# Optimization experiments

Measured on AMD Instinct MI355X. Metric: run time of the kernel, lower is better.

The kernel has to match this reference:

```python
import jax, jax.numpy as jnp
import numpy as np

N, E, IN, HID, H, G, OUT = 50000, 800000, 128, 96, 8, 64, 10
D = HID // H  # per-head dim = 12


def setup_inputs() -> dict:
    key = jax.random.key(0)
    ks = jax.random.split(key, 24)
    s = 0.1
    inp = {
        'x': jax.random.normal(ks[0], (N, IN), jnp.float32),
        'src': jax.random.randint(ks[1], (E,), 0, N, jnp.int32),
        'dst': jax.random.randint(ks[2], (E,), 0, N, jnp.int32),
        'graph_id': jax.random.randint(ks[3], (N,), 0, G, jnp.int32),
        # GraphConv layers (norm='both', weight + bias)
        'W1': jax.random.normal(ks[4], (IN, HID), jnp.float32) * s,
        'b1': jnp.zeros((HID,), jnp.float32),
        'W2': jax.random.normal(ks[5], (HID, HID), jnp.float32) * s,
        'b2': jnp.zeros((HID,), jnp.float32),
        # 3 GATv2 layers, stacked params
        'Ws': jax.random.normal(ks[6], (3, HID, HID), jnp.float32) * s,
        'bs': jnp.zeros((3, HID), jnp.float32),
        'Wd': jax.random.normal(ks[7], (3, HID, HID), jnp.float32) * s,
        'bd': jnp.zeros((3, HID), jnp.float32),
        'attn': jax.random.normal(ks[8], (3, H, D), jnp.float32) * s,
        # classifier MLP (dropout is identity at inference)
        'Wc1': jax.random.normal(ks[9], (HID, HID), jnp.float32) * s,
        'bc1': jnp.zeros((HID,), jnp.float32),
        'Wc2': jax.random.normal(ks[10], (HID, HID // 2), jnp.float32) * s,
        'bc2': jnp.zeros((HID // 2,), jnp.float32),
        'Wc3': jax.random.normal(ks[11], (HID // 2, OUT), jnp.float32) * s,
        'bc3': jnp.zeros((OUT,), jnp.float32),
    }
    return inp


def _graph_conv(h, W, b, src, dst):
    # DGL GraphConv, norm='both', allow_zero_in_degree (degrees clamped to >=1)
    ones = jnp.ones((E,), h.dtype)
    deg_out = jnp.clip(jax.ops.segment_sum(ones, src, N), 1.0)
    deg_in = jnp.clip(jax.ops.segment_sum(ones, dst, N), 1.0)
    h = (h * (deg_out ** -0.5)[:, None]) @ W          # [N, out]
    agg = jax.ops.segment_sum(h[src], dst, N)          # sum over in-edges
    return agg * (deg_in ** -0.5)[:, None] + b


def _gatv2(h, Ws, bs, Wd, bd, attn, src, dst):
    fs = (h @ Ws + bs).reshape(N, H, D)
    fd = (h @ Wd + bd).reshape(N, H, D)
    e = jax.nn.leaky_relu(fs[src] + fd[dst], 0.2)      # [E, H, D]
    logits = jnp.einsum('ehd,hd->eh', e, attn)         # [E, H]
    # edge softmax over incoming edges of each dst node
    m = jax.ops.segment_max(logits, dst, N)            # [N, H]
    ex = jnp.exp(logits - m[dst])
    den = jax.ops.segment_sum(ex, dst, N)              # [N, H]
    a = ex / den[dst]                                  # [E, H]
    rst = jax.ops.segment_sum(a[:, :, None] * fs[src], dst, N)  # [N, H, D]
    return jax.nn.relu(rst).reshape(N, HID)            # activation=relu, then view


def reference(x, src, dst, graph_id, W1, b1, W2, b2, Ws, bs, Wd, bd, attn,
              Wc1, bc1, Wc2, bc2, Wc3, bc3):
    h = jax.nn.relu(_graph_conv(x, W1, b1, src, dst))
    h = jax.nn.relu(_graph_conv(h, W2, b2, src, dst))
    for i in range(3):
        h = _gatv2(h, Ws[i], bs[i], Wd[i], bd[i], attn[i], src, dst)
    # dgl.max_nodes: per-graph max readout
    hg = jax.ops.segment_max(h, graph_id, G)           # [G, HID]
    z = jax.nn.relu(hg @ Wc1 + bc1)
    z = jax.nn.relu(z @ Wc2 + bc2)
    return z @ Wc3 + bc3                               # [G, OUT]
```

## Files before the change

kernel.cpp:

```cpp
#include <hip/hip_runtime.h>
#include <hip/hip_bf16.h>

#define Nn 50000
#define Ee 800000
#define INF_ 128
#define HIDF 96
#define HH 8
#define DD 12
#define GG 64
#define OUTF 10

#define SCAN_CHUNK 512
#define SCAN_BLOCKS ((Nn + SCAN_CHUNK - 1) / SCAN_CHUNK)
#define NSB ((Nn + 255) / 256)
#define RB 128

#define HCHK 256
#define HCHKE (Ee / HCHK)
#define NW 12512
#define DBIN 64

__global__ __launch_bounds__(512) void hist_lds(const int* __restrict__ src,
                                                const int* __restrict__ dst,
                                                unsigned int* __restrict__ partS,
                                                unsigned int* __restrict__ partD,
                                                unsigned char* __restrict__ edge_slot) {
    __shared__ unsigned int hS[NW];
    __shared__ unsigned int hD[NW];
    int b = blockIdx.x, t = threadIdx.x;
    for (int i = t; i < NW; i += 512) { hS[i] = 0u; hD[i] = 0u; }
    __syncthreads();
    int base = b * HCHKE;
    for (int i = t; i < HCHKE; i += 512) {
        int d = dst[base + i];
        unsigned int old = atomicAdd(&hD[d >> 2], 1u << ((d & 3) * 8));
        edge_slot[base + i] = (unsigned char)((old >> ((d & 3) * 8)) & 0xFFu);
        int s = src[base + i];
        atomicAdd(&hS[s >> 2], 1u << ((s & 3) * 8));
    }
    __syncthreads();
    for (int i = t; i < NW; i += 512) {
        partD[(size_t)b * NW + i] = hD[i];
        partS[(size_t)b * NW + i] = hS[i];
    }
}

__global__ __launch_bounds__(256) void hist_scan(unsigned int* __restrict__ partD,
                                                 const unsigned int* __restrict__ partS,
                                                 int* __restrict__ cnt_in,
                                                 float* __restrict__ degI_is,
                                                 float* __restrict__ degO_is,
                                                 int* __restrict__ dcnt) {
    __shared__ int hbin[DBIN];
    int t = threadIdx.x;
    if (t < DBIN) hbin[t] = 0;
    __syncthreads();
    int w = blockIdx.x * 256 + t;
    if (w < NW) {
        unsigned int run = 0u, totS = 0u;
        for (int b = 0; b < HCHK; ++b) {
            size_t idx = (size_t)b * NW + w;
            unsigned int v = partD[idx];
            partD[idx] = run;
            run += v;
            totS += partS[idx];
        }
#pragma unroll
        for (int j = 0; j < 4; ++j) {
            int k = w * 4 + j;
            if (k < Nn) {
                int di = (int)((run >> (j * 8)) & 0xFFu);
                int dо = (int)((totS >> (j * 8)) & 0xFFu);
                cnt_in[k] = di;
                degI_is[k] = rsqrtf((float)max(di, 1));
                degO_is[k] = rsqrtf((float)max(dо, 1));
                atomicAdd(&hbin[DBIN - 1 - min(di, DBIN - 1)], 1);
            }
        }
    }
    __syncthreads();
    if (t < DBIN && hbin[t]) atomicAdd(&dcnt[t], hbin[t]);
}

__global__ __launch_bounds__(256) void scan1_kernel(const int* __restrict__ cnt,
                                                    int* __restrict__ row_start,
                                                    int* __restrict__ blk_sum, int N) {
    __shared__ int part[256];
    int t = threadIdx.x;
    int base = blockIdx.x * SCAN_CHUNK;
    int i0 = base + 2 * t, i1 = i0 + 1;
    int a = (i0 < N) ? cnt[i0] : 0;
    int b = (i1 < N) ? cnt[i1] : 0;
    int s = a + b;
    part[t] = s;
    __syncthreads();
    for (int off = 1; off < 256; off <<= 1) {
        int v = (t >= off) ? part[t - off] : 0;
        __syncthreads();
        part[t] += v;
        __syncthreads();
    }
    int excl = part[t] - s;
    if (i0 < N) row_start[i0] = excl;
    if (i1 < N) row_start[i1] = excl + a;
    if (t == 255) blk_sum[blockIdx.x] = part[255];
}

__global__ __launch_bounds__(128) void scan2_kernel(const int* __restrict__ blk_sum,
                                                    int* __restrict__ blk_off,
                                                    int* __restrict__ row_start,
                                                    const int* __restrict__ dcnt,
                                                    int* __restrict__ dcur, int N) {
    __shared__ int part[128];
    int t = threadIdx.x;
    if (blockIdx.x == 0) {
        int v0 = (t < SCAN_BLOCKS) ? blk_sum[t] : 0;
        part[t] = v0;
        __syncthreads();
        for (int off = 1; off < 128; off <<= 1) {
            int v = (t >= off) ? part[t - off] : 0;
            __syncthreads();
            part[t] += v;
            __syncthreads();
        }
        blk_off[t] = part[t] - v0;
        if (t == 127) row_start[N] = part[127];
    } else {
        int v0 = (t < DBIN) ? dcnt[t] : 0;
        part[t] = v0;
        __syncthreads();
        for (int off = 1; off < DBIN; off <<= 1) {
            int v = (t >= off) ? part[t - off] : 0;
            __syncthreads();
            part[t] += v;
            __syncthreads();
        }
        if (t < DBIN) dcur[t] = part[t] - v0;
    }
}

__global__ __launch_bounds__(256) void scan3_kernel(int* __restrict__ row_start,
                                                    const int* __restrict__ blk_off,
                                                    const int* __restrict__ cnt_in,
                                                    int* __restrict__ dcur,
                                                    int* __restrict__ perm, int N) {
    int t = threadIdx.x;
    if (blockIdx.x < SCAN_BLOCKS) {
        int base = blockIdx.x * SCAN_CHUNK;
        int off = blk_off[blockIdx.x];
        int i0 = base + 2 * t, i1 = i0 + 1;
        if (i0 < N) row_start[i0] += off;
        if (i1 < N) row_start[i1] += off;
    } else {
        __shared__ int lh[DBIN];
        __shared__ int lbase[DBIN];
        if (t < DBIN) lh[t] = 0;
        __syncthreads();
        int n = (blockIdx.x - SCAN_BLOCKS) * 256 + t;
        int bin = 0, lslot = 0;
        if (n < N) {
            bin = DBIN - 1 - min(cnt_in[n], DBIN - 1);
            lslot = atomicAdd(&lh[bin], 1);
        }
        __syncthreads();
        if (t < DBIN) lbase[t] = lh[t] ? atomicAdd(&dcur[t], lh[t]) : 0;
        __syncthreads();
        if (n < N) perm[lbase[bin] + lslot] = n;
    }
}

__global__ __launch_bounds__(512) void fill_kernel(const int* __restrict__ src,
                                                   const int* __restrict__ dst,
                                                   const int* __restrict__ row_start,
                                                   const unsigned int* __restrict__ partD,
                                                   const unsigned char* __restrict__ edge_slot,
                                                   int* __restrict__ csr_src) {
    int b = blockIdx.x, t = threadIdx.x;
    int base = b * HCHKE;
    size_t po = (size_t)b * NW;
    for (int i = t; i < HCHKE; i += 512) {
        int e = base + i;
        int d = dst[e];
        int cb = (int)((partD[po + (d >> 2)] >> ((d & 3) * 8)) & 0xFFu);
        csr_src[row_start[d] + cb + (int)edge_slot[e]] = src[e];
    }
}

__global__ __launch_bounds__(192, 1) void gemm96(const float* __restrict__ A, int K,
                                                 const float* __restrict__ W,
                                                 const float* __restrict__ bias,
                                                 const float* __restrict__ rowScale,
                                                 float* __restrict__ out, int N) {
    __shared__ float W_lds[128 * 96];
    const int t = threadIdx.x;
    const int row0 = blockIdx.x * 64;
    const int tcol = t % 24;
    const int trow = t / 24;

    for (int i = t; i < K * 24; i += 192)
        ((float4*)W_lds)[i] = ((const float4*)W)[i];

    const float* Ap[8];
    float sc[8];
#pragma unroll
    for (int i = 0; i < 8; ++i) {
        int gr = row0 + trow + 8 * i;
        gr = gr < N ? gr : N - 1;
        Ap[i] = A + (size_t)gr * K;
        sc[i] = rowScale ? rowScale[gr] : 1.f;
    }
    float acc[8][4];
#pragma unroll
    for (int i = 0; i < 8; ++i)
#pragma unroll
        for (int j = 0; j < 4; ++j) acc[i][j] = 0.f;

    float4 bufA[8], bufB[8];
#pragma unroll
    for (int i = 0; i < 8; ++i) bufA[i] = *((const float4*)(Ap[i]));

    __syncthreads();

    auto compute = [&](const float4* a, int k) {
#pragma unroll
        for (int kk = 0; kk < 4; ++kk) {
            float4 wv = *((const float4*)(W_lds + (k + kk) * 96 + tcol * 4));
#pragma unroll
            for (int i = 0; i < 8; ++i) {
                float av = ((kk == 0) ? a[i].x : (kk == 1) ? a[i].y
                           : (kk == 2) ? a[i].z : a[i].w) * sc[i];
                acc[i][0] = fmaf(av, wv.x, acc[i][0]);
                acc[i][1] = fmaf(av, wv.y, acc[i][1]);
                acc[i][2] = fmaf(av, wv.z, acc[i][2]);
                acc[i][3] = fmaf(av, wv.w, acc[i][3]);
            }
        }
    };

    for (int k = 0; k + 8 <= K; k += 8) {
#pragma unroll
        for (int i = 0; i < 8; ++i) bufB[i] = *((const float4*)(Ap[i] + k + 4));
        compute(bufA, k);
        if (k + 8 < K) {
#pragma unroll
            for (int i = 0; i < 8; ++i) bufA[i] = *((const float4*)(Ap[i] + k + 8));
        }
        compute(bufB, k + 4);
    }
    float4 b4 = bias ? *((const float4*)(bias + tcol * 4)) : make_float4(0.f, 0.f, 0.f, 0.f);
#pragma unroll
    for (int i = 0; i < 8; ++i) {
        int gr = row0 + trow + 8 * i;
        if (gr < N) {
            float4 o = make_float4(acc[i][0] + b4.x, acc[i][1] + b4.y,
                                   acc[i][2] + b4.z, acc[i][3] + b4.w);
            *((float4*)(out + (size_t)gr * 96 + tcol * 4)) = o;
        }
    }
}

__global__ __launch_bounds__(192, 1) void gemm96x2(const float* __restrict__ A,
                                                   const float* __restrict__ W1_, const float* __restrict__ b1_,
                                                   const float* __restrict__ W2_, const float* __restrict__ b2_,
                                                   float* __restrict__ out1, float* __restrict__ out2, int N) {
    __shared__ float W_lds[2 * 96 * 96];
    const int t = threadIdx.x;
    const int row0 = blockIdx.x * 64;
    const int tcol = t % 24;
    const int trow = t / 24;

    for (int i = t; i < 96 * 24; i += 192) {
        ((float4*)W_lds)[i] = ((const float4*)W1_)[i];
        ((float4*)(W_lds + 96 * 96))[i] = ((const float4*)W2_)[i];
    }

    const float* Ap[8];
#pragma unroll
    for (int i = 0; i < 8; ++i) {
        int gr = row0 + trow + 8 * i;
        gr = gr < N ? gr : N - 1;
        Ap[i] = A + (size_t)gr * 96;
    }
    float acc1[8][4], acc2[8][4];
#pragma unroll
    for (int i = 0; i < 8; ++i)
#pragma unroll
        for (int j = 0; j < 4; ++j) { acc1[i][j] = 0.f; acc2[i][j] = 0.f; }

    float4 bufA[8], bufB[8];
#pragma unroll
    for (int i = 0; i < 8; ++i) bufA[i] = *((const float4*)(Ap[i]));

    __syncthreads();

    auto compute = [&](const float4* a, int k) {
#pragma unroll
        for (int kk = 0; kk < 4; ++kk) {
            float4 wv1 = *((const float4*)(W_lds + (k + kk) * 96 + tcol * 4));
            float4 wv2 = *((const float4*)(W_lds + 96 * 96 + (k + kk) * 96 + tcol * 4));
#pragma unroll
            for (int i = 0; i < 8; ++i) {
                float av = (kk == 0) ? a[i].x : (kk == 1) ? a[i].y : (kk == 2) ? a[i].z : a[i].w;
                acc1[i][0] = fmaf(av, wv1.x, acc1[i][0]);
                acc1[i][1] = fmaf(av, wv1.y, acc1[i][1]);
                acc1[i][2] = fmaf(av, wv1.z, acc1[i][2]);
                acc1[i][3] = fmaf(av, wv1.w, acc1[i][3]);
                acc2[i][0] = fmaf(av, wv2.x, acc2[i][0]);
                acc2[i][1] = fmaf(av, wv2.y, acc2[i][1]);
                acc2[i][2] = fmaf(av, wv2.z, acc2[i][2]);
                acc2[i][3] = fmaf(av, wv2.w, acc2[i][3]);
            }
        }
    };

    for (int k = 0; k + 8 <= 96; k += 8) {
#pragma unroll
        for (int i = 0; i < 8; ++i) bufB[i] = *((const float4*)(Ap[i] + k + 4));
        compute(bufA, k);
        if (k + 8 < 96) {
#pragma unroll
            for (int i = 0; i < 8; ++i) bufA[i] = *((const float4*)(Ap[i] + k + 8));
        }
        compute(bufB, k + 4);
    }
    float4 bb1 = *((const float4*)(b1_ + tcol * 4));
    float4 bb2 = *((const float4*)(b2_ + tcol * 4));
#pragma unroll
    for (int i = 0; i < 8; ++i) {
        int gr = row0 + trow + 8 * i;
        if (gr < N) {
            float4 o1 = make_float4(acc1[i][0] + bb1.x, acc1[i][1] + bb1.y,
                                    acc1[i][2] + bb1.z, acc1[i][3] + bb1.w);
            float4 o2 = make_float4(acc2[i][0] + bb2.x, acc2[i][1] + bb2.y,
                                    acc2[i][2] + bb2.z, acc2[i][3] + bb2.w);
            *((float4*)(out1 + (size_t)gr * 96 + tcol * 4)) = o1;
            *((float4*)(out2 + (size_t)gr * 96 + tcol * 4)) = o2;
        }
    }
}

__global__ __launch_bounds__(192) void gc_agg(const float* __restrict__ hW,
                                              const int* __restrict__ row_start,
                                              const int* __restrict__ csr_src,
                                              const float* __restrict__ degI_is,
                                              const float* __restrict__ bias,
                                              const int* __restrict__ perm,
                                              float* __restrict__ hout, int N) {
    int tid = blockIdx.x * 192 + threadIdx.x;
    int p = tid / 24;
    int c = (tid % 24) * 4;
    if (p >= N) return;
    int n = perm[p];
    int beg = row_start[n], end = row_start[n + 1];
    float4 s = make_float4(0.f, 0.f, 0.f, 0.f);
    int e = beg;
    for (; e + 4 <= end; e += 4) {
        int i0 = csr_src[e], i1 = csr_src[e + 1], i2 = csr_src[e + 2], i3 = csr_src[e + 3];
        float4 v0 = *(const float4*)(hW + (size_t)i0 * 96 + c);
        float4 v1 = *(const float4*)(hW + (size_t)i1 * 96 + c);
        float4 v2 = *(const float4*)(hW + (size_t)i2 * 96 + c);
        float4 v3 = *(const float4*)(hW + (size_t)i3 * 96 + c);
        s.x += (v0.x + v1.x) + (v2.x + v3.x);
        s.y += (v0.y + v1.y) + (v2.y + v3.y);
        s.z += (v0.z + v1.z) + (v2.z + v3.z);
        s.w += (v0.w + v1.w) + (v2.w + v3.w);
    }
    for (; e < end; ++e) {
        int i0 = csr_src[e];
        float4 v0 = *(const float4*)(hW + (size_t)i0 * 96 + c);
        s.x += v0.x; s.y += v0.y; s.z += v0.z; s.w += v0.w;
    }
    float dn = degI_is[n];
    float4 b = *(const float4*)(bias + c);
    float4 o;
    o.x = fmaxf(fmaf(s.x, dn, b.x), 0.f);
    o.y = fmaxf(fmaf(s.y, dn, b.y), 0.f);
    o.z = fmaxf(fmaf(s.z, dn, b.z), 0.f);
    o.w = fmaxf(fmaf(s.w, dn, b.w), 0.f);
    *(float4*)(hout + (size_t)n * 96 + c) = o;
}

__global__ __launch_bounds__(256) void gat_agg(const float* __restrict__ fs,
                                               const float* __restrict__ fd,
                                               const float* __restrict__ attn,
                                               const int* __restrict__ row_start,
                                               const int* __restrict__ csr_src,
                                               const int* __restrict__ perm,
                                               float* __restrict__ hout, int N) {
    int tid = blockIdx.x * 256 + threadIdx.x;
    int p = tid >> 3, hd = tid & 7;
    if (p >= N) return;
    int n = perm[p];
    float att[12], fdv[12];
    {
        const float4* ap = (const float4*)(attn + hd * 12);
        float4 a0 = ap[0], a1 = ap[1], a2 = ap[2];
        att[0]=a0.x; att[1]=a0.y; att[2]=a0.z; att[3]=a0.w;
        att[4]=a1.x; att[5]=a1.y; att[6]=a1.z; att[7]=a1.w;
        att[8]=a2.x; att[9]=a2.y; att[10]=a2.z; att[11]=a2.w;
        const float4* dp = (const float4*)(fd + (size_t)n * 96 + hd * 12);
        float4 d0 = dp[0], d1 = dp[1], d2 = dp[2];
        fdv[0]=d0.x; fdv[1]=d0.y; fdv[2]=d0.z; fdv[3]=d0.w;
        fdv[4]=d1.x; fdv[5]=d1.y; fdv[6]=d1.z; fdv[7]=d1.w;
        fdv[8]=d2.x; fdv[9]=d2.y; fdv[10]=d2.z; fdv[11]=d2.w;
    }
    int beg = row_start[n], end = row_start[n + 1];
    float m0 = -3.0e38f, den0 = 0.f, m1 = -3.0e38f, den1 = 0.f;
    float A0[12], A1[12];
#pragma unroll
    for (int d = 0; d < 12; ++d) { A0[d] = 0.f; A1[d] = 0.f; }

    auto proc = [&](const float4& s0, const float4& s1, const float4& s2,
                    float& m, float& den, float* acc) {
        float fsv[12];
        fsv[0]=s0.x; fsv[1]=s0.y; fsv[2]=s0.z; fsv[3]=s0.w;
        fsv[4]=s1.x; fsv[5]=s1.y; fsv[6]=s1.z; fsv[7]=s1.w;
        fsv[8]=s2.x; fsv[9]=s2.y; fsv[10]=s2.z; fsv[11]=s2.w;
        float logit = 0.f;
#pragma unroll
        for (int d = 0; d < 12; ++d) {
            float u = fsv[d] + fdv[d];
            u = u > 0.f ? u : 0.2f * u;
            logit = fmaf(u, att[d], logit);
        }
        float nm = fmaxf(m, logit);
        float cc = __expf(m - nm);
        float w  = __expf(logit - nm);
        den = fmaf(den, cc, w);
#pragma unroll
        for (int d = 0; d < 12; ++d) acc[d] = fmaf(acc[d], cc, w * fsv[d]);
        m = nm;
    };

    int e = beg;
    for (; e + 4 <= end; e += 4) {
        int i0 = csr_src[e], i1 = csr_src[e + 1], i2 = csr_src[e + 2], i3 = csr_src[e + 3];
        const float4* p0 = (const float4*)(fs + (size_t)i0 * 96 + hd * 12);
        const float4* p1 = (const float4*)(fs + (size_t)i1 * 96 + hd * 12);
        const float4* p2 = (const float4*)(fs + (size_t)i2 * 96 + hd * 12);
        const float4* p3 = (const float4*)(fs + (size_t)i3 * 96 + hd * 12);
        float4 a0 = p0[0], a1 = p0[1], a2 = p0[2];
        float4 b0 = p1[0], b1 = p1[1], b2 = p1[2];
        float4 c0 = p2[0], c1 = p2[1], c2 = p2[2];
        float4 d0 = p3[0], d1 = p3[1], d2 = p3[2];
        proc(a0, a1, a2, m0, den0, A0);
        proc(b0, b1, b2, m1, den1, A1);
        proc(c0, c1, c2, m0, den0, A0);
        proc(d0, d1, d2, m1, den1, A1);
    }
    for (; e < end; ++e) {
        int i0 = csr_src[e];
        const float4* p0 = (const float4*)(fs + (size_t)i0 * 96 + hd * 12);
        float4 a0 = p0[0], a1 = p0[1], a2 = p0[2];
        proc(a0, a1, a2, m0, den0, A0);
    }
    float nm = fmaxf(m0, m1);
    float c0 = __expf(m0 - nm), c1 = __expf(m1 - nm);
    float den = den0 * c0 + den1 * c1;
    float inv = den > 0.f ? 1.f / den : 0.f;
    float* op = hout + (size_t)n * 96 + hd * 12;
#pragma unroll
    for (int d = 0; d < 12; ++d)
        op[d] = fmaxf((A0[d] * c0 + A1[d] * c1) * inv, 0.f);
}

__global__ __launch_bounds__(384) void readout_partial(const float* __restrict__ h,
                                                       const int* __restrict__ graph_id,
                                                       float* __restrict__ partial, int N) {
    __shared__ int lhg[GG * 96];
    int t = threadIdx.x;
    for (int i = t; i < GG * 96; i += 384) lhg[i] = 0;
    __syncthreads();
    int f = t % 96, nl = t / 96;
    for (int n0 = blockIdx.x * 4; n0 < N; n0 += RB * 4) {
        int n = n0 + nl;
        if (n < N) {
            int g = graph_id[n];
            float v = h[(size_t)n * 96 + f];
            atomicMax(&lhg[g * 96 + f], __float_as_int(v));
        }
    }
    __syncthreads();
    for (int i = t; i < GG * 96; i += 384)
        partial[(size_t)blockIdx.x * (GG * 96) + i] = __int_as_float(lhg[i]);
}

__global__ void readout_reduce(const float* __restrict__ partial, float* __restrict__ hg) {
    int i = blockIdx.x * 256 + threadIdx.x;
    if (i < GG * 96) {
        float m = 0.f;
        for (int b = 0; b < RB; ++b) m = fmaxf(m, partial[(size_t)b * (GG * 96) + i]);
        hg[i] = m;
    }
}

__global__ __launch_bounds__(96) void mlp_kernel(const float* __restrict__ hg,
                                                 const float* __restrict__ Wc1, const float* __restrict__ bc1,
                                                 const float* __restrict__ Wc2, const float* __restrict__ bc2,
                                                 const float* __restrict__ Wc3, const float* __restrict__ bc3,
                                                 float* __restrict__ out) {
    int g = blockIdx.x;
    int t = threadIdx.x;
    __shared__ float z0[96], z1[96], z2[48];
    z0[t] = hg[(size_t)g * 96 + t];
    __syncthreads();
    float s = bc1[t];
    for (int k = 0; k < 96; ++k) s = fmaf(z0[k], Wc1[k * 96 + t], s);
    z1[t] = fmaxf(s, 0.f);
    __syncthreads();
    if (t < 48) {
        float s2 = bc2[t];
        for (int k = 0; k < 96; ++k) s2 = fmaf(z1[k], Wc2[k * 48 + t], s2);
        z2[t] = fmaxf(s2, 0.f);
    }
    __syncthreads();
    if (t < 10) {
        float s3 = bc3[t];
        for (int k = 0; k < 48; ++k) s3 = fmaf(z2[k], Wc3[k * 10 + t], s3);
        out[(size_t)g * 10 + t] = s3;
    }
}

extern "C" void kernel_launch(void* const* d_in, const int* in_sizes, int n_in,
                              void* d_out, int out_size, void* d_ws, size_t ws_size,
                              hipStream_t stream) {
    const float* x        = (const float*)d_in[0];
    const int*   src      = (const int*)d_in[1];
    const int*   dst      = (const int*)d_in[2];
    const int*   graph_id = (const int*)d_in[3];
    const float* W1  = (const float*)d_in[4];
    const float* b1  = (const float*)d_in[5];
    const float* W2  = (const float*)d_in[6];
    const float* b2  = (const float*)d_in[7];
    const float* Ws  = (const float*)d_in[8];
    const float* bs  = (const float*)d_in[9];
    const float* Wd  = (const float*)d_in[10];
    const float* bd  = (const float*)d_in[11];
    const float* attn = (const float*)d_in[12];
    const float* Wc1 = (const float*)d_in[13];
    const float* bc1 = (const float*)d_in[14];
    const float* Wc2 = (const float*)d_in[15];
    const float* bc2 = (const float*)d_in[16];
    const float* Wc3 = (const float*)d_in[17];
    const float* bc3 = (const float*)d_in[18];
    float* out = (float*)d_out;

    char* ws = (char*)d_ws;
    size_t off = 0;
    auto alloc = [&](size_t bytes) {
        char* p = ws + off;
        off = (off + bytes + 255) & ~(size_t)255;
        return p;
    };
    int*   cnt_in    = (int*)alloc(Nn * 4);
    int*   row_start = (int*)alloc((Nn + 1) * 4);
    unsigned char* edge_slot = (unsigned char*)alloc(Ee);
    int*   csr_src   = (int*)alloc(Ee * 4);
    int*   perm      = (int*)alloc(Nn * 4);
    float* degI_is   = (float*)alloc(Nn * 4);
    float* degO_is   = (float*)alloc(Nn * 4);
    float* bufH      = (float*)alloc((size_t)Nn * 96 * 4);
    float* bufT      = (float*)alloc((size_t)Nn * 96 * 4);
    float* bufFd     = (float*)alloc((size_t)Nn * 96 * 4);
    float* hg        = (float*)alloc(GG * 96 * 4);
    float* partial   = (float*)alloc((size_t)RB * GG * 96 * 4);
    int*   blk_sum   = (int*)alloc(128 * 4);
    int*   blk_off   = (int*)alloc(128 * 4);
    int*   dcnt      = (int*)alloc(DBIN * 4);
    int*   dcur      = (int*)alloc(DBIN * 4);

    unsigned int* partS = (unsigned int*)bufT;
    unsigned int* partD = (unsigned int*)bufFd;

    hipMemsetAsync(dcnt, 0, DBIN * 4, stream);

    hist_lds<<<HCHK, 512, 0, stream>>>(src, dst, partS, partD, edge_slot);
    hist_scan<<<(NW + 255) / 256, 256, 0, stream>>>(partD, partS, cnt_in, degI_is, degO_is, dcnt);
    scan1_kernel<<<SCAN_BLOCKS, 256, 0, stream>>>(cnt_in, row_start, blk_sum, Nn);
    scan2_kernel<<<2, 128, 0, stream>>>(blk_sum, blk_off, row_start, dcnt, dcur, Nn);
    scan3_kernel<<<SCAN_BLOCKS + NSB, 256, 0, stream>>>(row_start, blk_off, cnt_in, dcur, perm, Nn);
    fill_kernel<<<HCHK, 512, 0, stream>>>(src, dst, row_start, partD, edge_slot, csr_src);

    int gemm_blocks = (Nn + 63) / 64;
    int agg_blocks  = (Nn * 24 + 191) / 192;
    int gat_blocks  = (Nn * 8 + 255) / 256;

    gemm96<<<gemm_blocks, 192, 0, stream>>>(x, 128, W1, nullptr, degO_is, bufT, Nn);
    gc_agg<<<agg_blocks, 192, 0, stream>>>(bufT, row_start, csr_src, degI_is, b1, perm, bufH, Nn);
    gemm96<<<gemm_blocks, 192, 0, stream>>>(bufH, 96, W2, nullptr, degO_is, bufT, Nn);
    gc_agg<<<agg_blocks, 192, 0, stream>>>(bufT, row_start, csr_src, degI_is, b2, perm, bufH, Nn);

    for (int l = 0; l < 3; ++l) {
        const float* Wsl = Ws + (size_t)l * 96 * 96;
        const float* bsl = bs + (size_t)l * 96;
        const float* Wdl = Wd + (size_t)l * 96 * 96;
        const float* bdl = bd + (size_t)l * 96;
        const float* atl = attn + (size_t)l * 96;
        gemm96x2<<<gemm_blocks, 192, 0, stream>>>(bufH, Wsl, bsl, Wdl, bdl, bufT, bufFd, Nn);
        gat_agg<<<gat_blocks, 256, 0, stream>>>(bufT, bufFd, atl, row_start, csr_src, perm, bufH, Nn);
    }

    readout_partial<<<RB, 384, 0, stream>>>(bufH, graph_id, partial, Nn);
    readout_reduce<<<(GG * 96 + 255) / 256, 256, 0, stream>>>(partial, hg);
    mlp_kernel<<<GG, 96, 0, stream>>>(hg, Wc1, bc1, Wc2, bc2, Wc3, bc3, out);
}
```

Before: 645.7 us.

## Split GAT edge aggregation across four lanes per head with shuffle merge

The GATv2 aggregation kernel now assigns four threads per (node, head) instead of one. Each lane walks every fourth in-edge with its own online-softmax state, and the partial max, denominator and accumulators are merged with xor shuffles. Each lane then writes three of the twelve output features. This raises thread-level parallelism and memory-level parallelism for the gather, in exchange for 4x more threads that each redundantly load attn/fd and do shuffle reductions, and less per-thread unrolling of the edge loop.

```diff
diff --git a/kernel.cpp b/kernel.cpp
--- a/kernel.cpp
+++ b/kernel.cpp
@@ -388,7 +388,9 @@
                                                const int* __restrict__ perm,
                                                float* __restrict__ hout, int N) {
     int tid = blockIdx.x * 256 + threadIdx.x;
-    int p = tid >> 3, hd = tid & 7;
+    int p = tid >> 5;
+    int hd = (tid >> 2) & 7;
+    int q = tid & 3;
     if (p >= N) return;
     int n = perm[p];
     float att[12], fdv[12];
@@ -405,13 +407,15 @@
         fdv[8]=d2.x; fdv[9]=d2.y; fdv[10]=d2.z; fdv[11]=d2.w;
     }
     int beg = row_start[n], end = row_start[n + 1];
-    float m0 = -3.0e38f, den0 = 0.f, m1 = -3.0e38f, den1 = 0.f;
-    float A0[12], A1[12];
-#pragma unroll
-    for (int d = 0; d < 12; ++d) { A0[d] = 0.f; A1[d] = 0.f; }
-
-    auto proc = [&](const float4& s0, const float4& s1, const float4& s2,
-                    float& m, float& den, float* acc) {
+    float m = -3.0e38f, den = 0.f;
+    float A[12];
+#pragma unroll
+    for (int d = 0; d < 12; ++d) A[d] = 0.f;
+
+    for (int e = beg + q; e < end; e += 4) {
+        int i0 = csr_src[e];
+        const float4* p0 = (const float4*)(fs + (size_t)i0 * 96 + hd * 12);
+        float4 s0 = p0[0], s1 = p0[1], s2 = p0[2];
         float fsv[12];
         fsv[0]=s0.x; fsv[1]=s0.y; fsv[2]=s0.z; fsv[3]=s0.w;
         fsv[4]=s1.x; fsv[5]=s1.y; fsv[6]=s1.z; fsv[7]=s1.w;
@@ -428,40 +432,36 @@
         float w  = __expf(logit - nm);
         den = fmaf(den, cc, w);
 #pragma unroll
-        for (int d = 0; d < 12; ++d) acc[d] = fmaf(acc[d], cc, w * fsv[d]);
+        for (int d = 0; d < 12; ++d) A[d] = fmaf(A[d], cc, w * fsv[d]);
         m = nm;
-    };
-
-    int e = beg;
-    for (; e + 4 <= end; e += 4) {
-        int i0 = csr_src[e], i1 = csr_src[e + 1], i2 = csr_src[e + 2], i3 = csr_src[e + 3];
-        const float4* p0 = (const float4*)(fs + (size_t)i0 * 96 + hd * 12);
-        const float4* p1 = (const float4*)(fs + (size_t)i1 * 96 + hd * 12);
-        const float4* p2 = (const float4*)(fs + (size_t)i2 * 96 + hd * 12);
-        const float4* p3 = (const float4*)(fs + (size_t)i3 * 96 + hd * 12);
-        float4 a0 = p0[0], a1 = p0[1], a2 = p0[2];
-        float4 b0 = p1[0], b1 = p1[1], b2 = p1[2];
-        float4 c0 = p2[0], c1 = p2[1], c2 = p2[2];
-        float4 d0 = p3[0], d1 = p3[1], d2 = p3[2];
-        proc(a0, a1, a2, m0, den0, A0);
-        proc(b0, b1, b2, m1, den1, A1);
-        proc(c0, c1, c2, m0, den0, A0);
-        proc(d0, d1, d2, m1, den1, A1);
-    }
-    for (; e < end; ++e) {
-        int i0 = csr_src[e];
-        const float4* p0 = (const float4*)(fs + (size_t)i0 * 96 + hd * 12);
-        float4 a0 = p0[0], a1 = p0[1], a2 = p0[2];
-        proc(a0, a1, a2, m0, den0, A0);
-    }
-    float nm = fmaxf(m0, m1);
-    float c0 = __expf(m0 - nm), c1 = __expf(m1 - nm);
-    float den = den0 * c0 + den1 * c1;
+    }
+
+#pragma unroll
+    for (int off = 1; off <= 2; off <<= 1) {
+        float m2   = __shfl_xor(m, off, 64);
+        float den2 = __shfl_xor(den, off, 64);
+        float nm = fmaxf(m, m2);
+        float c1 = __expf(m - nm);
+        float c2 = __expf(m2 - nm);
+        den = den * c1 + den2 * c2;
+#pragma unroll
+        for (int d = 0; d < 12; ++d) {
+            float a2 = __shfl_xor(A[d], off, 64);
+            A[d] = A[d] * c1 + a2 * c2;
+        }
+        m = nm;
+    }
+
     float inv = den > 0.f ? 1.f / den : 0.f;
     float* op = hout + (size_t)n * 96 + hd * 12;
 #pragma unroll
-    for (int d = 0; d < 12; ++d)
-        op[d] = fmaxf((A0[d] * c0 + A1[d] * c1) * inv, 0.f);
+    for (int j = 0; j < 3; ++j) {
+        int d = q * 3 + j;
+        float v = (d == 0) ? A[0] : (d == 1) ? A[1] : (d == 2) ? A[2] : (d == 3) ? A[3]
+                : (d == 4) ? A[4] : (d == 5) ? A[5] : (d == 6) ? A[6] : (d == 7) ? A[7]
+                : (d == 8) ? A[8] : (d == 9) ? A[9] : (d == 10) ? A[10] : A[11];
+        op[d] = fmaxf(v * inv, 0.f);
+    }
 }
 
 __global__ __launch_bounds__(384) void readout_partial(const float* __restrict__ h,
@@ -583,7 +583,7 @@
 
     int gemm_blocks = (Nn + 63) / 64;
     int agg_blocks  = (Nn * 24 + 191) / 192;
-    int gat_blocks  = (Nn * 8 + 255) / 256;
+    int gat_blocks  = (Nn * 32 + 255) / 256;
 
     gemm96<<<gemm_blocks, 192, 0, stream>>>(x, 128, W1, nullptr, degO_is, bufT, Nn);
     gc_agg<<<agg_blocks, 192, 0, stream>>>(bufT, row_start, csr_src, degI_is, b1, perm, bufH, Nn);
```

Result: no change. 640.0 us (-0.9%).
